# Kernel tuning notes

Hardware: AMD Instinct MI355X
Metric: run time of the kernel (lower is better)

The kernel has to match this reference:

```python
import jax, jax.numpy as jnp
import numpy as np
import math

D_MODEL = 512
EXPAND = 2
D_INNER = EXPAND * D_MODEL          # 1024
HEADDIM = 8
NHEADS = D_INNER // HEADDIM         # 128
NGROUPS = 2
D_STATE = 16
CONV_DIM = D_INNER + 2 * NGROUPS * D_STATE   # 1088
D_IN_PROJ = 2 * D_INNER + 2 * NGROUPS * D_STATE + NHEADS  # 2240
P13 = [(0, 0), (1, 1)]
P31 = [(1, 1), (0, 0)]
P33 = [(1, 1), (1, 1)]


def silu(x):
    return x * jax.nn.sigmoid(x)


def dwconv(x, w, pad):
    # depthwise 2D conv; x: (B,C,H,W), w: (C,1,kh,kw)
    return jax.lax.conv_general_dilated(
        x, w, (1, 1), pad,
        dimension_numbers=('NCHW', 'OIHW', 'NCHW'),
        feature_group_count=x.shape[1])


def interleave_ch(a, b):
    # channel-interleave: out[:, ::2] = a, out[:, 1::2] = b
    Bn, C, Hh, Ww = a.shape
    return jnp.stack([a, b], axis=2).reshape(Bn, 2 * C, Hh, Ww)


def linear_attn(x, dt, A, Bm, Cm, Dp):
    # non-causal linear-attention duality of Mamba2 (grouped heads)
    # x: (B,L,h,p), dt: (B,L,h), A: (h,) negative, Bm/Cm: (B,L,g*ds), Dp: (h,)
    b, L, h, p = x.shape
    g, ds = NGROUPS, D_STATE
    dA = -(dt * A[None, None, :])          # ssd_positive_dA -> positive
    Vs = x * dA[..., None]
    K = Bm.reshape(b, L, g, ds)
    Q = Cm.reshape(b, L, g, ds)
    Vg = Vs.reshape(b, L, h // g, g, p)
    KV = jnp.einsum('blgs,blmgp->bmgsp', K, Vg)       # (b, h/g, g, ds, p)
    y = jnp.einsum('blgs,bmgsp->blmgp', Q, KV)        # (b, L, h/g, g, p)
    y = y + (x * Dp[None, None, :, None]).reshape(b, L, h // g, g, p)
    return y.reshape(b, L, h, p)


def setup_inputs() -> dict:
    key = jax.random.key(0)
    ks = jax.random.split(key, 20)
    Bn, Hh, Ww = 8, 64, 64
    L = Hh * Ww
    u = jax.random.normal(ks[0], (Bn, L, D_MODEL), jnp.float32)
    W_in = jax.random.normal(ks[1], (D_IN_PROJ, D_MODEL), jnp.float32) / math.sqrt(D_MODEL)
    dt = jnp.exp(jax.random.uniform(ks[2], (NHEADS,)) * (math.log(0.1) - math.log(0.001)) + math.log(0.001))
    dt = jnp.clip(dt, 1e-4, None)
    dt_bias = dt + jnp.log(-jnp.expm1(-dt))
    A_log = jnp.log(jax.random.uniform(ks[3], (NHEADS,), minval=1.0, maxval=16.0))
    Dp = jnp.ones((NHEADS,), jnp.float32)

    def cw(k, c, kh, kw):
        return jax.random.normal(k, (c, 1, kh, kw), jnp.float32) / math.sqrt(kh * kw)

    bcC = 2 * NGROUPS * D_STATE // 4  # 16
    w_conv2d = cw(ks[4], CONV_DIM // 2, 3, 3)
    w13x1 = cw(ks[5], D_INNER // 4, 1, 3)
    w31x1 = cw(ks[6], D_INNER // 4, 3, 1)
    w13x2 = cw(ks[7], D_INNER // 4, 1, 3)
    w31x2 = cw(ks[8], D_INNER // 4, 3, 1)
    w13bc1 = cw(ks[9], bcC, 1, 3)
    w31bc1 = cw(ks[10], bcC, 3, 1)
    w13bc2 = cw(ks[11], bcC, 1, 3)
    w31bc2 = cw(ks[12], bcC, 3, 1)
    w_conv2d_z = cw(ks[13], D_INNER, 3, 3)
    ln_g = jnp.ones((D_INNER,), jnp.float32)
    ln_b = jnp.zeros((D_INNER,), jnp.float32)
    scale = jnp.float32(1.0)
    shift = jnp.float32(0.0)
    alpha1 = jnp.float32(1.0)
    alpha2 = jnp.float32(1.0)
    W_out = jax.random.normal(ks[14], (D_MODEL, 2 * D_INNER), jnp.float32) / math.sqrt(2 * D_INNER)
    return dict(u=u, H=Hh, W=Ww, W_in=W_in, dt_bias=dt_bias, A_log=A_log, Dp=Dp,
                w_conv2d=w_conv2d, w13x1=w13x1, w31x1=w31x1, w13x2=w13x2, w31x2=w31x2,
                w13bc1=w13bc1, w31bc1=w31bc1, w13bc2=w13bc2, w31bc2=w31bc2,
                w_conv2d_z=w_conv2d_z, ln_g=ln_g, ln_b=ln_b, scale=scale, shift=shift,
                alpha1=alpha1, alpha2=alpha2, W_out=W_out)


def reference(u, H, W, W_in, dt_bias, A_log, Dp, w_conv2d, w13x1, w31x1, w13x2, w31x2,
              w13bc1, w31bc1, w13bc2, w31bc2, w_conv2d_z, ln_g, ln_b, scale, shift,
              alpha1, alpha2, W_out):
    Bn, L, _ = u.shape
    zxbcdt = u @ W_in.T                                 # (B,L,2240)
    z = zxbcdt[..., :D_INNER]
    xBC = zxbcdt[..., D_INNER:D_INNER + CONV_DIM]
    dt = zxbcdt[..., D_INNER + CONV_DIM:]
    dt = jax.nn.softplus(dt + dt_bias)                  # (B,L,h)

    # even/odd channel-interleave split, reshape to NCHW feature maps
    even = xBC[..., 0::2].reshape(Bn, H, W, -1).transpose(0, 3, 1, 2)
    odd = xBC[..., 1::2].reshape(Bn, H, W, -1).transpose(0, 3, 1, 2)
    even = silu(dwconv(even, w_conv2d, P33))

    oe = odd[:, 0::2]
    oo = odd[:, 1::2]
    x_oe, bc_oe = oe[:, :D_INNER // 4], oe[:, D_INNER // 4:]
    x_oo, bc_oo = oo[:, :D_INNER // 4], oo[:, D_INNER // 4:]
    x_oe = silu(dwconv(dwconv(x_oe, w31x1, P31), w13x1, P13))
    x_oo = silu(dwconv(dwconv(x_oo, w13x2, P13), w31x2, P31))
    bc_oe = silu(dwconv(dwconv(bc_oe, w13bc1, P13), w31bc1, P31))
    bc_oo = silu(dwconv(dwconv(bc_oo, w31bc2, P31), w13bc2, P13))
    xbc_oe = jnp.concatenate([x_oe, bc_oe], axis=1)
    xbc_oo = jnp.concatenate([x_oo, bc_oo], axis=1)
    odd = interleave_ch(xbc_oe, xbc_oo)

    xBCc = interleave_ch(even, odd)                     # (B, CONV_DIM, H, W)
    xBCc = xBCc.transpose(0, 2, 3, 1).reshape(Bn, L, CONV_DIM)
    x = xBCc[..., :D_INNER]
    Bm = xBCc[..., D_INNER:D_INNER + NGROUPS * D_STATE]
    Cm = xBCc[..., D_INNER + NGROUPS * D_STATE:]

    A = -jnp.exp(A_log)
    y = linear_attn(x.reshape(Bn, L, NHEADS, HEADDIM), dt, A, Bm, Cm, Dp)
    y = y.reshape(Bn, L, D_INNER)

    mu = y.mean(-1, keepdims=True)
    var = ((y - mu) ** 2).mean(-1, keepdims=True)
    y = (y - mu) / jnp.sqrt(var + 1e-5) * ln_g + ln_b
    y = y * scale + shift

    zc = z.reshape(Bn, H, W, D_INNER).transpose(0, 3, 1, 2)
    zc = silu(dwconv(zc, w_conv2d_z, P33))
    zc = zc.transpose(0, 2, 3, 1).reshape(Bn, L, D_INNER)

    out = jnp.concatenate([alpha1 * y, alpha2 * zc], axis=-1) @ W_out.T
    return out
```

## Files before the change

### kernel.cpp

```cpp
#include <hip/hip_runtime.h>
#include <hip/hip_bf16.h>
#include <cstdint>
#include <cstddef>

#define HDIM    64
#define WDIM    64
#define LPB     4096
#define DMODEL  512
#define DIN     1024
#define CONVD   1088
#define DPROJ   2240
#define NHEADS  128
#define NCV     2112

using f16    = _Float16;
using f16x4  = __attribute__((ext_vector_type(4))) _Float16;
using f16x8  = __attribute__((ext_vector_type(8))) _Float16;
using f32x4  = __attribute__((ext_vector_type(4))) float;

#define VM_CNT(n) asm volatile("s_waitcnt vmcnt(" #n ")" ::: "memory")
#define LDSFENCE  asm volatile("" ::: "memory")

__device__ __forceinline__ float siluf(float x) { return x / (1.f + __expf(-x)); }
__device__ __forceinline__ float fsilu(float x) {
  return x * __builtin_amdgcn_rcpf(1.f + __expf(-x));
}

__device__ __forceinline__ void fma_mix_lo(float& acc, unsigned a, unsigned b) {
  asm("v_fma_mix_f32 %0, %1, %2, %0 op_sel_hi:[1,1,0]" : "+v"(acc) : "v"(a), "v"(b));
}
__device__ __forceinline__ void fma_mix_hi(float& acc, unsigned a, unsigned b) {
  asm("v_fma_mix_f32 %0, %1, %2, %0 op_sel:[1,1,0] op_sel_hi:[1,1,0]" : "+v"(acc) : "v"(a), "v"(b));
}
__device__ __forceinline__ void fmixl(float& acc, unsigned a, float b) {
  asm("v_fma_mix_f32 %0, %1, %2, %0 op_sel_hi:[1,0,0]" : "+v"(acc) : "v"(a), "v"(b));
}
__device__ __forceinline__ void fmixh(float& acc, unsigned a, float b) {
  asm("v_fma_mix_f32 %0, %1, %2, %0 op_sel:[1,0,0] op_sel_hi:[1,0,0]" : "+v"(acc) : "v"(a), "v"(b));
}
__device__ __forceinline__ void fma8(float* acc, const uint4& v, const uint4& w) {
  fma_mix_lo(acc[0], v.x, w.x);  fma_mix_hi(acc[1], v.x, w.x);
  fma_mix_lo(acc[2], v.y, w.y);  fma_mix_hi(acc[3], v.y, w.y);
  fma_mix_lo(acc[4], v.z, w.z);  fma_mix_hi(acc[5], v.z, w.z);
  fma_mix_lo(acc[6], v.w, w.w);  fma_mix_hi(acc[7], v.w, w.w);
}

__global__ __launch_bounds__(256) void k_cvt(const float* __restrict__ in, f16* __restrict__ out) {
  size_t i = ((size_t)blockIdx.x * 256 + threadIdx.x) * 4;
  f32x4 v = *(const f32x4*)(in + i);
  f16x4 o;
  #pragma unroll
  for (int j = 0; j < 4; ++j) o[j] = (f16)v[j];
  *(f16x4*)(out + i) = o;
}

__global__ __launch_bounds__(256) void k_cvt_win(const float* __restrict__ W, f16* __restrict__ out) {
  int i = blockIdx.x * 256 + threadIdx.x;
  int row = i >> 9, col = i & 511;
  float v = (row < DPROJ) ? W[row * 512 + col] : 0.f;
  out[i] = (f16)v;
}

__global__ __launch_bounds__(256) void k_keff(const float* __restrict__ w33,
                       const float* __restrict__ w13x1, const float* __restrict__ w31x1,
                       const float* __restrict__ w13x2, const float* __restrict__ w31x2,
                       const float* __restrict__ w13bc1, const float* __restrict__ w31bc1,
                       const float* __restrict__ w13bc2, const float* __restrict__ w31bc2,
                       const float* __restrict__ wz,
                       f16* __restrict__ keffall) {
  int j = blockIdx.x * 256 + threadIdx.x;
  if (j >= NCV) return;
  if (j < 1024) {
    #pragma unroll
    for (int tap = 0; tap < 9; ++tap) keffall[tap * NCV + j] = (f16)wz[j * 9 + tap];
    return;
  }
  int jj = j - 1024;
  float kh[3] = {0,0,0}, kw[3] = {0,0,0};
  bool dense = ((jj & 1) == 0);
  if (!dense) {
    int m = jj >> 2;
    if ((jj & 3) == 1) {
      if (m < 256) { for (int t=0;t<3;++t){ kh[t]=w31x1[m*3+t];  kw[t]=w13x1[m*3+t];  } }
      else { int q=m-256; for (int t=0;t<3;++t){ kh[t]=w31bc1[q*3+t]; kw[t]=w13bc1[q*3+t]; } }
    } else {
      if (m < 256) { for (int t=0;t<3;++t){ kh[t]=w31x2[m*3+t];  kw[t]=w13x2[m*3+t];  } }
      else { int q=m-256; for (int t=0;t<3;++t){ kh[t]=w31bc2[q*3+t]; kw[t]=w13bc2[q*3+t]; } }
    }
  }
  #pragma unroll
  for (int dh = 0; dh < 3; ++dh)
    #pragma unroll
    for (int dw = 0; dw < 3; ++dw) {
      float v = dense ? w33[(jj >> 1) * 9 + dh*3 + dw] : kh[dh] * kw[dw];
      keffall[(dh*3 + dw) * NCV + j] = (f16)v;
    }
}

__global__ __launch_bounds__(512, 1) void k_gemm8(const f16* __restrict__ A, int lda,
                                                  const f16* __restrict__ Bm, int ldb,
                                                  f16* __restrict__ C, int ldc,
                                                  int K, int NW, int ntn) {
  __shared__ __align__(16) f16 Al[2 * 16384];
  __shared__ __align__(16) f16 Bl[2 * 16384];

  int nwg = gridDim.x, bid = blockIdx.x;
  int q = nwg >> 3, r = nwg & 7;
  int xcd = bid & 7, loc = bid >> 3;
  int wg  = (xcd < r ? xcd * (q + 1) : r * (q + 1) + (xcd - r) * q) + loc;
  long m0 = (long)(wg / ntn) * 256;
  long n0 = (long)(wg % ntn) * 256;

  const int tid  = threadIdx.x;
  const int wid  = tid >> 6, lane = tid & 63;
  const int wr   = wid >> 2, wc = wid & 3;

  const int rowoff = wid * 8 + (lane >> 3);
  const int scolS  = ((lane & 7) ^ (lane >> 3)) * 8;
  const int ldst   = wid * 512;

  const int fr   = lane & 15;
  const int koff = (lane >> 4) * 8;
  const int swz8 = (lane & 7) << 3;

  f32x4 acc[8][4];
  #pragma unroll
  for (int i = 0; i < 8; ++i)
    #pragma unroll
    for (int j = 0; j < 4; ++j) acc[i][j] = (f32x4){0.f,0.f,0.f,0.f};

  const int NT = K >> 6;

  auto stA = [&](int par, int X, int kb) {
    __builtin_amdgcn_global_load_lds(
      (const __attribute__((address_space(1))) void*)(A + (m0 + X*64 + rowoff) * (long)lda + kb + scolS),
      (__attribute__((address_space(3))) void*)&Al[par*16384 + X*4096 + ldst], 16, 0, 0);
  };
  auto stB = [&](int par, int X, int kb) {
    __builtin_amdgcn_global_load_lds(
      (const __attribute__((address_space(1))) void*)(Bm + (n0 + X*64 + rowoff) * (long)ldb + kb + scolS),
      (__attribute__((address_space(3))) void*)&Bl[par*16384 + X*4096 + ldst], 16, 0, 0);
  };

  stB(0,0,0); stB(0,1,0); stB(0,2,0); stB(0,3,0);
  stA(0,0,0); stA(0,2,0); stA(0,1,0); stA(0,3,0);

  for (int t = 0; t < NT; ++t) {
    const bool last = (t == NT - 1);
    const int pr = t & 1, pw = (t + 1) & 1;
    const int kb = (t + 1) << 6;
    const f16* Ard = &Al[pr * 16384];
    const f16* Brd = &Bl[pr * 16384];
    f16x8 bf[4][2];

    #pragma unroll
    for (int s = 0; s < 4; ++s) {
      f16x8 af[2][2];
      if (s == 1 || s == 3) {
        #pragma unroll
        for (int j = 0; j < 2; ++j)
          #pragma unroll
          for (int k = 0; k < 2; ++k) {
            int rr = wr*128 + (2*s + j)*16 + fr;
            af[j][k] = *(const f16x8*)&Ard[rr*64 + ((k*32 + koff) ^ swz8)];
          }
      }
      if (!last) {
        if (s == 0)      { stB(pw, 0, kb); stB(pw, 1, kb); }
        else if (s == 1) { stB(pw, 2, kb); stB(pw, 3, kb); }
        else if (s == 2) { stA(pw, 0, kb); stA(pw, 2, kb); }
        else             { stA(pw, 1, kb); stA(pw, 3, kb); }
      }
      if (s == 0) { if (!last) { VM_CNT(4); } else { VM_CNT(2); } }
      if (s == 2) { if (!last) { VM_CNT(6); } else { VM_CNT(0); } }
      __builtin_amdgcn_s_barrier();
      LDSFENCE;
      if (s == 0) {
        #pragma unroll
        for (int ni = 0; ni < 4; ++ni)
          #pragma unroll
          for (int k = 0; k < 2; ++k) {
            int rr = wc*64 + ni*16 + fr;
            bf[ni][k] = *(const f16x8*)&Brd[rr*64 + ((k*32 + koff) ^ swz8)];
          }
      }
      if (s == 0 || s == 2) {
        #pragma unroll
        for (int j = 0; j < 2; ++j)
          #pragma unroll
          for (int k = 0; k < 2; ++k) {
            int rr = wr*128 + (2*s + j)*16 + fr;
            af[j][k] = *(const f16x8*)&Ard[rr*64 + ((k*32 + koff) ^ swz8)];
          }
      }
      __builtin_amdgcn_s_setprio(1);
      #pragma unroll
      for (int j = 0; j < 2; ++j)
        #pragma unroll
        for (int ni = 0; ni < 4; ++ni)
          #pragma unroll
          for (int k = 0; k < 2; ++k)
            acc[2*s + j][ni] = __builtin_amdgcn_mfma_f32_16x16x32_f16(af[j][k], bf[ni][k], acc[2*s + j][ni], 0, 0, 0);
      __builtin_amdgcn_s_setprio(0);
      __builtin_amdgcn_s_barrier();
      LDSFENCE;
    }
  }

  const int cr = (lane >> 4) * 4;
  const int cc = lane & 15;
  #pragma unroll
  for (int mi = 0; mi < 8; ++mi) {
    long rbase = m0 + wr*128 + mi*16 + cr;
    #pragma unroll
    for (int ni = 0; ni < 4; ++ni) {
      int col = (int)n0 + wc*64 + ni*16 + cc;
      if (col < NW) {
        f16* cp = C + rbase * (long)ldc + col;
        #pragma unroll
        for (int rr2 = 0; rr2 < 4; ++rr2) cp[(long)rr2 * ldc] = (f16)acc[mi][ni][rr2];
      }
    }
  }
}

template<typename OutT>
__global__ __launch_bounds__(256) void k_gemmf(const f16* __restrict__ A, int lda,
                                               const f16* __restrict__ Bm, int ldb,
                                               OutT* __restrict__ C, int ldc,
                                               int Kseg, int NW, int ntn, int ntmn, long Cseg) {
  __shared__ __align__(16) f16 As[128 * 32];
  __shared__ __align__(16) f16 Bs[128 * 32];

  int nwg = gridDim.x, bid = blockIdx.x;
  int q = nwg >> 3, r = nwg & 7;
  int xcd = bid & 7, loc = bid >> 3;
  int wg  = (xcd < r ? xcd * (q + 1) : r * (q + 1) + (xcd - r) * q) + loc;
  int kseg = wg / ntmn;
  int rem  = wg - kseg * ntmn;
  long m0 = (long)(rem / ntn) * 128;
  long n0 = (long)(rem % ntn) * 128;
  const int kbase = kseg * Kseg;

  const int tid  = threadIdx.x;
  const int w    = tid >> 6, lane = tid & 63;
  const int wr   = w >> 1, wc = w & 1;

  f32x4 acc[4][4];
  #pragma unroll
  for (int i = 0; i < 4; ++i)
    #pragma unroll
    for (int j = 0; j < 4; ++j) acc[i][j] = (f32x4){0.f,0.f,0.f,0.f};

  const int srow = w * 16 + (lane >> 2);
  const int scol = (lane & 3) * 8;
  const long aoff = (m0 + srow) * (long)lda + scol + kbase;
  const long boff = (n0 + srow) * (long)ldb + scol + kbase;
  const int fr = lane & 15;
  const int kc = (lane >> 4) * 8;

  for (int k0 = 0; k0 < Kseg; k0 += 32) {
    #pragma unroll
    for (int i = 0; i < 2; ++i) {
      long ao = aoff + (long)i*64*lda + k0;
      long bo = boff + (long)i*64*ldb + k0;
      int ls = (i*4 + w) * 512;
      __builtin_amdgcn_global_load_lds((const __attribute__((address_space(1))) void*)(A + ao),
                                       (__attribute__((address_space(3))) void*)&As[ls], 16, 0, 0);
      __builtin_amdgcn_global_load_lds((const __attribute__((address_space(1))) void*)(Bm + bo),
                                       (__attribute__((address_space(3))) void*)&Bs[ls], 16, 0, 0);
    }
    __syncthreads();
    f16x8 af[4], bf[4];
    #pragma unroll
    for (int f = 0; f < 4; ++f) {
      af[f] = *(const f16x8*)&As[(wr*64 + f*16 + fr) * 32 + kc];
      bf[f] = *(const f16x8*)&Bs[(wc*64 + f*16 + fr) * 32 + kc];
    }
    #pragma unroll
    for (int i = 0; i < 4; ++i)
      #pragma unroll
      for (int j = 0; j < 4; ++j)
        acc[i][j] = __builtin_amdgcn_mfma_f32_16x16x32_f16(af[i], bf[j], acc[i][j], 0, 0, 0);
    __syncthreads();
  }

  OutT* Cb = C + (long)kseg * Cseg;
  const int cr = (lane >> 4) * 4;
  const int cc = lane & 15;
  #pragma unroll
  for (int i = 0; i < 4; ++i) {
    long rbase = m0 + wr*64 + i*16 + cr;
    #pragma unroll
    for (int j = 0; j < 4; ++j) {
      int col = (int)n0 + wc*64 + j*16 + cc;
      if (col < NW) {
        OutT* cp = Cb + rbase * (long)ldc + col;
        #pragma unroll
        for (int r2 = 0; r2 < 4; ++r2) cp[(long)r2 * ldc] = (OutT)acc[i][j][r2];
      }
    }
  }
}

__global__ __launch_bounds__(256) void k_red2h(const f16* __restrict__ part, long seg,
                                               float* __restrict__ out) {
  long i = ((long)blockIdx.x * 256 + threadIdx.x) * 4;
  f16x4 s0 = *(const f16x4*)(part + i);
  f16x4 s1 = *(const f16x4*)(part + seg + i);
  f32x4 o;
  #pragma unroll
  for (int j = 0; j < 4; ++j) o[j] = (float)s0[j] + (float)s1[j];
  *(f32x4*)(out + i) = o;
}

__global__ __launch_bounds__(192) void k_conv_all(const f16* __restrict__ zx,
                                                  const f16* __restrict__ keffall,
                                                  const float* __restrict__ a2_p,
                                                  const float* __restrict__ dt_bias,
                                                  const float* __restrict__ A_log,
                                                  f16* __restrict__ xbc,
                                                  f16* __restrict__ g2,
                                                  float* __restrict__ dAb) {
  int t = threadIdx.x;
  int bid = blockIdx.x, qq = gridDim.x >> 3;
  int grp = (bid & 7) * qq + (bid >> 3);
  int l0 = grp * 2;
  long lb = (long)(l0 & ~(LPB - 1));
  int h  = (l0 >> 6) & 63;
  int w0 = l0 & 63;

  if (t < 132) {
    int c0 = t * 8;
    int c1 = c0 + 1056;
    float a00[8] = {0,0,0,0,0,0,0,0};
    float a01[8] = {0,0,0,0,0,0,0,0};
    float a10[8] = {0,0,0,0,0,0,0,0};
    float a11[8] = {0,0,0,0,0,0,0,0};
    const uint4 z4 = {0u,0u,0u,0u};

    #pragma unroll
    for (int dh = 0; dh < 3; ++dh) {
      int hh = h + dh - 1;
      if (hh < 0 || hh >= HDIM) continue;
      const f16* rp = zx + (lb + (long)(hh * 64)) * DPROJ;
      uint4 v0[4], v1[4];
      #pragma unroll
      for (int pp = 0; pp < 4; ++pp) {
        int ww = w0 + pp - 1;
        ww = ww < 0 ? 0 : (ww > 63 ? 63 : ww);
        const f16* tp = rp + (long)ww * DPROJ;
        v0[pp] = *(const uint4*)(tp + c0);
        v1[pp] = *(const uint4*)(tp + c1);
      }
      if (w0 == 0)  { v0[0] = z4; v1[0] = z4; }
      if (w0 == 62) { v0[3] = z4; v1[3] = z4; }
      #pragma unroll
      for (int dw = 0; dw < 3; ++dw) {
        uint4 wa = *(const uint4*)&keffall[(dh*3 + dw) * NCV + c0];
        uint4 wb = *(const uint4*)&keffall[(dh*3 + dw) * NCV + c1];
        fma8(a00, v0[dw],     wa);
        fma8(a10, v0[dw + 1], wa);
        fma8(a01, v1[dw],     wb);
        fma8(a11, v1[dw + 1], wb);
      }
    }

    float a2 = a2_p[0];
    #pragma unroll
    for (int ti = 0; ti < 2; ++ti) {
      long l = l0 + ti;
      const float* pc0 = ti ? a10 : a00;
      const float* pc1 = ti ? a11 : a01;
      f16x8 o8;
      if (c0 < 1024) {
        #pragma unroll
        for (int j = 0; j < 8; ++j) o8[j] = (f16)(a2 * fsilu(pc0[j]));
        *(f16x8*)&g2[l * 2048 + 1024 + c0] = o8;
      } else {
        #pragma unroll
        for (int j = 0; j < 8; ++j) o8[j] = (f16)fsilu(pc0[j]);
        *(f16x8*)&xbc[l * (long)CONVD + (c0 - 1024)] = o8;
      }
      f16x8 o9;
      #pragma unroll
      for (int j = 0; j < 8; ++j) o9[j] = (f16)fsilu(pc1[j]);
      *(f16x8*)&xbc[l * (long)CONVD + (c1 - 1024)] = o9;
    }
  } else if (t < 164) {
    int idx = t - 132;
    int ti = idx >> 4;
    int hd = (idx & 15) * 8;
    long l = l0 + ti;
    f16x8 x = *(const f16x8*)&zx[l * (long)DPROJ + NCV + hd];
    f32x4 o0, o1;
    #pragma unroll
    for (int j = 0; j < 8; ++j) {
      float xx = (float)x[j] + dt_bias[hd + j];
      float sp = (xx > 20.f) ? xx : log1pf(__expf(xx));
      float dv = sp * __expf(A_log[hd + j]);
      if (j < 4) o0[j] = dv; else o1[j-4] = dv;
    }
    *(f32x4*)&dAb[l * 128 + hd]     = o0;
    *(f32x4*)&dAb[l * 128 + hd + 4] = o1;
  }
}

__global__ __launch_bounds__(512) void k_kv_part(const f16* __restrict__ xbc,
                                                 const float* __restrict__ dA,
                                                 float* __restrict__ part) {
  int t = threadIdx.x;
  int m = t >> 3, p = t & 7;
  int lc = blockIdx.x, b = blockIdx.y;
  float acc0[16], acc1[16];
  #pragma unroll
  for (int s = 0; s < 16; ++s) { acc0[s] = 0.f; acc1[s] = 0.f; }
  long lbase = (long)b * LPB + lc * 64;
  for (int li = 0; li < 64; li += 2) {
    long row = lbase + li;
    const f16* xr0 = xbc + row * CONVD;
    const f16* xr1 = xr0 + CONVD;
    float2 aa0 = *(const float2*)&dA[row * 128 + 2*m];
    float2 aa1 = *(const float2*)&dA[(row + 1) * 128 + 2*m];
    f16 x00s = xr0[16*m + p],     x01s = xr0[16*m + 8 + p];
    f16 x10s = xr1[16*m + p],     x11s = xr1[16*m + 8 + p];
    uint4 q00 = *(const uint4*)(xr0 + DIN);
    uint4 q01 = *(const uint4*)(xr0 + DIN + 8);
    uint4 q02 = *(const uint4*)(xr0 + DIN + 16);
    uint4 q03 = *(const uint4*)(xr0 + DIN + 24);
    uint4 q10 = *(const uint4*)(xr1 + DIN);
    uint4 q11 = *(const uint4*)(xr1 + DIN + 8);
    uint4 q12 = *(const uint4*)(xr1 + DIN + 16);
    uint4 q13 = *(const uint4*)(xr1 + DIN + 24);
    float xv00 = (float)x00s * aa0.x, xv01 = (float)x01s * aa0.y;
    float xv10 = (float)x10s * aa1.x, xv11 = (float)x11s * aa1.y;
    unsigned a00[4] = {q00.x, q00.y, q00.z, q00.w};
    unsigned a01[4] = {q01.x, q01.y, q01.z, q01.w};
    unsigned a02[4] = {q02.x, q02.y, q02.z, q02.w};
    unsigned a03[4] = {q03.x, q03.y, q03.z, q03.w};
    unsigned a10[4] = {q10.x, q10.y, q10.z, q10.w};
    unsigned a11[4] = {q11.x, q11.y, q11.z, q11.w};
    unsigned a12[4] = {q12.x, q12.y, q12.z, q12.w};
    unsigned a13[4] = {q13.x, q13.y, q13.z, q13.w};
    #pragma unroll
    for (int k = 0; k < 4; ++k) {
      fmixl(acc0[2*k],   a00[k], xv00);  fmixh(acc0[2*k+1],   a00[k], xv00);
      fmixl(acc0[8+2*k], a01[k], xv00);  fmixh(acc0[8+2*k+1], a01[k], xv00);
      fmixl(acc1[2*k],   a02[k], xv01);  fmixh(acc1[2*k+1],   a02[k], xv01);
      fmixl(acc1[8+2*k], a03[k], xv01);  fmixh(acc1[8+2*k+1], a03[k], xv01);
      fmixl(acc0[2*k],   a10[k], xv10);  fmixh(acc0[2*k+1],   a10[k], xv10);
      fmixl(acc0[8+2*k], a11[k], xv10);  fmixh(acc0[8+2*k+1], a11[k], xv10);
      fmixl(acc1[2*k],   a12[k], xv11);  fmixh(acc1[2*k+1],   a12[k], xv11);
      fmixl(acc1[8+2*k], a13[k], xv11);  fmixh(acc1[8+2*k+1], a13[k], xv11);
    }
  }
  long base = ((long)(b*64 + lc)) * 16384 + (long)m * 256;
  #pragma unroll
  for (int s = 0; s < 16; ++s) {
    part[base + s*8 + p]       = acc0[s];
    part[base + 128 + s*8 + p] = acc1[s];
  }
}

__global__ __launch_bounds__(256) void k_kv_red(const float* __restrict__ part,
                                                float* __restrict__ KV) {
  int e4 = (blockIdx.x * 256 + threadIdx.x) * 4;
  int b = blockIdx.y;
  f32x4 s = (f32x4){0.f,0.f,0.f,0.f};
  #pragma unroll 4
  for (int lc = 0; lc < 64; ++lc) {
    f32x4 v = *(const f32x4*)&part[((long)(b*64 + lc)) * 16384 + e4];
    #pragma unroll
    for (int j = 0; j < 4; ++j) s[j] += v[j];
  }
  *(f32x4*)&KV[(long)b * 16384 + e4] = s;
}

__global__ __launch_bounds__(256) void k_y_ln(const f16* __restrict__ xbc,
                                              const float* __restrict__ KV,
                                              const float* __restrict__ Dp,
                                              const float* __restrict__ ln_g,
                                              const float* __restrict__ ln_b,
                                              const float* __restrict__ sc_p,
                                              const float* __restrict__ sh_p,
                                              const float* __restrict__ a1_p,
                                              f16* __restrict__ g2) {
  __shared__ float Qs[64][32];
  __shared__ float red[2][2][8];
  int t = threadIdx.x;
  int hd = t >> 1, pb = (t & 1) * 4;
  int m = hd >> 1, g = hd & 1;
  int b = blockIdx.x >> 6;
  long l0 = (long)b * LPB + (blockIdx.x & 63) * 64;

  f32x4 kv[16];
  #pragma unroll
  for (int s = 0; s < 16; ++s)
    kv[s] = *(const f32x4*)&KV[(long)b * 16384 + m*256 + g*128 + s*8 + pb];

  {
    int tok = t >> 2, q8 = (t & 3) * 8;
    f16x8 qv = *(const f16x8*)&xbc[(l0 + tok) * CONVD + 1056 + q8];
    #pragma unroll
    for (int j = 0; j < 8; ++j) Qs[tok][q8 + j] = (float)qv[j];
  }
  int c0 = hd*8 + pb;
  f32x4 lg = *(const f32x4*)&ln_g[c0];
  f32x4 lb = *(const f32x4*)&ln_b[c0];
  float dpv = Dp[hd];
  float sc = sc_p[0], sh = sh_p[0], a1 = a1_p[0];
  int wv = t >> 6, lane = t & 63;
  __syncthreads();

  for (int tok = 0; tok < 64; tok += 2) {
    int par = (tok >> 1) & 1;
    long row0 = l0 + tok, row1 = row0 + 1;
    f16x4 xa = *(const f16x4*)&xbc[row0 * CONVD + c0];
    f16x4 xb = *(const f16x4*)&xbc[row1 * CONVD + c0];
    f32x4 ya, yb;
    #pragma unroll
    for (int j = 0; j < 4; ++j) { ya[j] = (float)xa[j] * dpv; yb[j] = (float)xb[j] * dpv; }
    #pragma unroll
    for (int s = 0; s < 16; ++s) {
      float qa = Qs[tok][g*16 + s];
      float qb = Qs[tok + 1][g*16 + s];
      #pragma unroll
      for (int j = 0; j < 4; ++j) {
        ya[j] = fmaf(qa, kv[s][j], ya[j]);
        yb[j] = fmaf(qb, kv[s][j], yb[j]);
      }
    }
    float s1a = ya[0]+ya[1]+ya[2]+ya[3];
    float s2a = ya[0]*ya[0]+ya[1]*ya[1]+ya[2]*ya[2]+ya[3]*ya[3];
    float s1b = yb[0]+yb[1]+yb[2]+yb[3];
    float s2b = yb[0]*yb[0]+yb[1]*yb[1]+yb[2]*yb[2]+yb[3]*yb[3];
    #pragma unroll
    for (int off = 1; off < 64; off <<= 1) {
      s1a += __shfl_xor(s1a, off, 64);
      s2a += __shfl_xor(s2a, off, 64);
      s1b += __shfl_xor(s1b, off, 64);
      s2b += __shfl_xor(s2b, off, 64);
    }
    if (lane == 0) {
      red[par][0][wv*2] = s1a;  red[par][0][wv*2 + 1] = s2a;
      red[par][1][wv*2] = s1b;  red[par][1][wv*2 + 1] = s2b;
    }
    __syncthreads();
    #pragma unroll
    for (int ti = 0; ti < 2; ++ti) {
      const float* rr = red[par][ti];
      float S1 = rr[0] + rr[2] + rr[4] + rr[6];
      float S2 = rr[1] + rr[3] + rr[5] + rr[7];
      float mu   = S1 * (1.f/1024.f);
      float var  = S2 * (1.f/1024.f) - mu*mu;
      float rstd = rsqrtf(var + 1e-5f);
      f32x4& yv = ti ? yb : ya;
      f16x4 o4;
      #pragma unroll
      for (int j = 0; j < 4; ++j) {
        float yn = (yv[j] - mu) * rstd * lg[j] + lb[j];
        o4[j] = (f16)(a1 * (yn * sc + sh));
      }
      *(f16x4*)&g2[(l0 + tok + ti) * 2048 + c0] = o4;
    }
  }
}

extern "C" void kernel_launch(void* const* d_in, const int* in_sizes, int n_in,
                              void* d_out, int out_size, void* d_ws, size_t ws_size,
                              hipStream_t stream) {
  const float* u       = (const float*)d_in[0];
  const float* W_in    = (const float*)d_in[3];
  const float* dt_bias = (const float*)d_in[4];
  const float* A_log   = (const float*)d_in[5];
  const float* Dp      = (const float*)d_in[6];
  const float* w33     = (const float*)d_in[7];
  const float* w13x1   = (const float*)d_in[8];
  const float* w31x1   = (const float*)d_in[9];
  const float* w13x2   = (const float*)d_in[10];
  const float* w31x2   = (const float*)d_in[11];
  const float* w13bc1  = (const float*)d_in[12];
  const float* w31bc1  = (const float*)d_in[13];
  const float* w13bc2  = (const float*)d_in[14];
  const float* w31bc2  = (const float*)d_in[15];
  const float* wz      = (const float*)d_in[16];
  const float* ln_g    = (const float*)d_in[17];
  const float* ln_b    = (const float*)d_in[18];
  const float* sc      = (const float*)d_in[19];
  const float* sh      = (const float*)d_in[20];
  const float* a1      = (const float*)d_in[21];
  const float* a2      = (const float*)d_in[22];
  const float* W_out   = (const float*)d_in[23];

  const size_t B_G2   = 16777216;
  const size_t B_ZX   = 18350080;
  const size_t B_XBC  = 8912896;
  const size_t B_DA   = 2097152;
  const size_t B_KV   = 65536;
  const size_t perC   = B_G2 + B_ZX + B_XBC + B_DA + B_KV;
  const size_t persist = 2359296 + 2097152 + 38912;

  int C = 8;
  while (C > 1 && persist + (size_t)C * perC > ws_size) C >>= 1;
  const int nch = 8 / C;
  const int Mc  = C * LPB;

  char* p = (char*)d_ws;
  f16*   win_f   = (f16*)p;   p += 2359296;
  f16*   wout_f  = (f16*)p;   p += 2097152;
  f16*   keffall = (f16*)p;   p += 38912;
  char*  arena   = p;
  f16*   g2      = (f16*)arena;
  f16*   u_f     = (f16*)arena;
  p = arena + (size_t)C * B_G2;
  f16*   zx      = (f16*)p;   p += (size_t)C * B_ZX;
  f16*   xbc     = (f16*)p;   p += (size_t)C * B_XBC;
  float* dAb     = (float*)p; p += (size_t)C * B_DA;
  float* KV      = (float*)p; p += (size_t)C * B_KV;
  float* part   = (float*)zx;
  f16*   kpart  = (f16*)zx;

  k_cvt_win<<<4608, 256, 0, stream>>>(W_in, win_f);
  k_cvt    <<<1024, 256, 0, stream>>>(W_out, wout_f);
  k_keff   <<<9, 256, 0, stream>>>(w33, w13x1, w31x1, w13x2, w31x2,
                                   w13bc1, w31bc1, w13bc2, w31bc2, wz, keffall);

  for (int ch = 0; ch < nch; ++ch) {
    const float* uc   = u + (size_t)ch * Mc * 512;
    float*       outc = (float*)d_out + (size_t)ch * Mc * 512;
    const int ntm = Mc / 128;

    k_cvt<<<Mc/2, 256, 0, stream>>>(uc, u_f);

    k_gemm8<<<(Mc/256)*9, 512, 0, stream>>>(u_f, 512, win_f, 512,
                                            zx, DPROJ, 512, DPROJ, 9);

    k_conv_all<<<Mc/2, 192, 0, stream>>>(zx, keffall, a2, dt_bias, A_log,
                                         xbc, g2, dAb);

    k_kv_part <<<dim3(64, C), 512, 0, stream>>>(xbc, dAb, part);
    k_kv_red  <<<dim3(16, C), 256, 0, stream>>>(part, KV);
    k_y_ln    <<<C*64, 256, 0, stream>>>(xbc, KV, Dp, ln_g, ln_b, sc, sh, a1, g2);

    const long cseg = (long)Mc * 512;
    k_gemmf<f16><<<ntm*4*2, 256, 0, stream>>>(g2, 2048, wout_f, 2048,
                                              kpart, 512, 1024, 512, 4, ntm*4, cseg);
    k_red2h<<<Mc/2, 256, 0, stream>>>(kpart, cseg, outc);
  }
}
```

Before: 546.6 us.

## Fuse fp32-to-fp16 input conversion into a smaller-tile in-projection GEMM

Drops the separate pass that converts the fp32 input u to fp16. The in-projection GEMM now loads fp32 A tiles straight into LDS and converts them to fp16 in registers before the MFMAs. The large 256x256 tile, double-buffered, software-pipelined kernel is replaced by a simple 128x128 single-buffered kernel with K-step 32 and two barriers per step. This saves one extra read and write of the activations, but loses the load/compute overlap, doubles A traffic by loading fp32, and adds conversion work in the inner loop.

```diff
diff --git a/kernel.cpp b/kernel.cpp
--- a/kernel.cpp
+++ b/kernel.cpp
@@ -17,9 +17,6 @@
 using f16x4  = __attribute__((ext_vector_type(4))) _Float16;
 using f16x8  = __attribute__((ext_vector_type(8))) _Float16;
 using f32x4  = __attribute__((ext_vector_type(4))) float;
-
-#define VM_CNT(n) asm volatile("s_waitcnt vmcnt(" #n ")" ::: "memory")
-#define LDSFENCE  asm volatile("" ::: "memory")
 
 __device__ __forceinline__ float siluf(float x) { return x / (1.f + __expf(-x)); }
 __device__ __forceinline__ float fsilu(float x) {
@@ -97,128 +94,81 @@
     }
 }
 
-__global__ __launch_bounds__(512, 1) void k_gemm8(const f16* __restrict__ A, int lda,
-                                                  const f16* __restrict__ Bm, int ldb,
-                                                  f16* __restrict__ C, int ldc,
-                                                  int K, int NW, int ntn) {
-  __shared__ __align__(16) f16 Al[2 * 16384];
-  __shared__ __align__(16) f16 Bl[2 * 16384];
+__global__ __launch_bounds__(256) void k_gemm1c(const float* __restrict__ A,
+                                                const f16* __restrict__ Bm, int ldb,
+                                                f16* __restrict__ C, int ldc,
+                                                int K, int NW, int ntn) {
+  __shared__ __align__(16) float As[128 * 32];
+  __shared__ __align__(16) f16   Bs[128 * 32];
 
   int nwg = gridDim.x, bid = blockIdx.x;
   int q = nwg >> 3, r = nwg & 7;
   int xcd = bid & 7, loc = bid >> 3;
   int wg  = (xcd < r ? xcd * (q + 1) : r * (q + 1) + (xcd - r) * q) + loc;
-  long m0 = (long)(wg / ntn) * 256;
-  long n0 = (long)(wg % ntn) * 256;
+  long m0 = (long)(wg / ntn) * 128;
+  long n0 = (long)(wg % ntn) * 128;
 
   const int tid  = threadIdx.x;
-  const int wid  = tid >> 6, lane = tid & 63;
-  const int wr   = wid >> 2, wc = wid & 3;
-
-  const int rowoff = wid * 8 + (lane >> 3);
-  const int scolS  = ((lane & 7) ^ (lane >> 3)) * 8;
-  const int ldst   = wid * 512;
-
+  const int w    = tid >> 6, lane = tid & 63;
+  const int wr   = w >> 1, wc = w & 1;
+
+  f32x4 acc[4][4];
+  #pragma unroll
+  for (int i = 0; i < 4; ++i)
+    #pragma unroll
+    for (int j = 0; j < 4; ++j) acc[i][j] = (f32x4){0.f,0.f,0.f,0.f};
+
+  const int arow = tid >> 3;
+  const int acol = (tid & 7) * 4;
+  const int brow = w * 16 + (lane >> 2);
+  const int bcol = (lane & 3) * 8;
   const int fr   = lane & 15;
-  const int koff = (lane >> 4) * 8;
-  const int swz8 = (lane & 7) << 3;
-
-  f32x4 acc[8][4];
-  #pragma unroll
-  for (int i = 0; i < 8; ++i)
-    #pragma unroll
-    for (int j = 0; j < 4; ++j) acc[i][j] = (f32x4){0.f,0.f,0.f,0.f};
-
-  const int NT = K >> 6;
-
-  auto stA = [&](int par, int X, int kb) {
-    __builtin_amdgcn_global_load_lds(
-      (const __attribute__((address_space(1))) void*)(A + (m0 + X*64 + rowoff) * (long)lda + kb + scolS),
-      (__attribute__((address_space(3))) void*)&Al[par*16384 + X*4096 + ldst], 16, 0, 0);
-  };
-  auto stB = [&](int par, int X, int kb) {
-    __builtin_amdgcn_global_load_lds(
-      (const __attribute__((address_space(1))) void*)(Bm + (n0 + X*64 + rowoff) * (long)ldb + kb + scolS),
-      (__attribute__((address_space(3))) void*)&Bl[par*16384 + X*4096 + ldst], 16, 0, 0);
-  };
-
-  stB(0,0,0); stB(0,1,0); stB(0,2,0); stB(0,3,0);
-  stA(0,0,0); stA(0,2,0); stA(0,1,0); stA(0,3,0);
-
-  for (int t = 0; t < NT; ++t) {
-    const bool last = (t == NT - 1);
-    const int pr = t & 1, pw = (t + 1) & 1;
-    const int kb = (t + 1) << 6;
-    const f16* Ard = &Al[pr * 16384];
-    const f16* Brd = &Bl[pr * 16384];
-    f16x8 bf[4][2];
-
-    #pragma unroll
-    for (int s = 0; s < 4; ++s) {
-      f16x8 af[2][2];
-      if (s == 1 || s == 3) {
-        #pragma unroll
-        for (int j = 0; j < 2; ++j)
-          #pragma unroll
-          for (int k = 0; k < 2; ++k) {
-            int rr = wr*128 + (2*s + j)*16 + fr;
-            af[j][k] = *(const f16x8*)&Ard[rr*64 + ((k*32 + koff) ^ swz8)];
-          }
-      }
-      if (!last) {
-        if (s == 0)      { stB(pw, 0, kb); stB(pw, 1, kb); }
-        else if (s == 1) { stB(pw, 2, kb); stB(pw, 3, kb); }
-        else if (s == 2) { stA(pw, 0, kb); stA(pw, 2, kb); }
-        else             { stA(pw, 1, kb); stA(pw, 3, kb); }
-      }
-      if (s == 0) { if (!last) { VM_CNT(4); } else { VM_CNT(2); } }
-      if (s == 2) { if (!last) { VM_CNT(6); } else { VM_CNT(0); } }
-      __builtin_amdgcn_s_barrier();
-      LDSFENCE;
-      if (s == 0) {
-        #pragma unroll
-        for (int ni = 0; ni < 4; ++ni)
-          #pragma unroll
-          for (int k = 0; k < 2; ++k) {
-            int rr = wc*64 + ni*16 + fr;
-            bf[ni][k] = *(const f16x8*)&Brd[rr*64 + ((k*32 + koff) ^ swz8)];
-          }
-      }
-      if (s == 0 || s == 2) {
-        #pragma unroll
-        for (int j = 0; j < 2; ++j)
-          #pragma unroll
-          for (int k = 0; k < 2; ++k) {
-            int rr = wr*128 + (2*s + j)*16 + fr;
-            af[j][k] = *(const f16x8*)&Ard[rr*64 + ((k*32 + koff) ^ swz8)];
-          }
-      }
-      __builtin_amdgcn_s_setprio(1);
-      #pragma unroll
-      for (int j = 0; j < 2; ++j)
-        #pragma unroll
-        for (int ni = 0; ni < 4; ++ni)
-          #pragma unroll
-          for (int k = 0; k < 2; ++k)
-            acc[2*s + j][ni] = __builtin_amdgcn_mfma_f32_16x16x32_f16(af[j][k], bf[ni][k], acc[2*s + j][ni], 0, 0, 0);
-      __builtin_amdgcn_s_setprio(0);
-      __builtin_amdgcn_s_barrier();
-      LDSFENCE;
-    }
+  const int kc   = (lane >> 4) * 8;
+
+  for (int k0 = 0; k0 < K; k0 += 32) {
+    #pragma unroll
+    for (int i = 0; i < 4; ++i) {
+      __builtin_amdgcn_global_load_lds(
+        (const __attribute__((address_space(1))) void*)(A + (m0 + i*32 + arow) * 512L + acol + k0),
+        (__attribute__((address_space(3))) void*)&As[(i*256 + tid) * 4], 16, 0, 0);
+    }
+    #pragma unroll
+    for (int i = 0; i < 2; ++i) {
+      __builtin_amdgcn_global_load_lds(
+        (const __attribute__((address_space(1))) void*)(Bm + (n0 + i*64 + brow) * (long)ldb + bcol + k0),
+        (__attribute__((address_space(3))) void*)&Bs[(i*4 + w) * 512], 16, 0, 0);
+    }
+    __syncthreads();
+    f16x8 af[4], bf[4];
+    #pragma unroll
+    for (int f = 0; f < 4; ++f) {
+      int rr = wr*64 + f*16 + fr;
+      f32x4 a0 = *(const f32x4*)&As[rr*32 + kc];
+      f32x4 a1 = *(const f32x4*)&As[rr*32 + kc + 4];
+      #pragma unroll
+      for (int j = 0; j < 4; ++j) { af[f][j] = (f16)a0[j]; af[f][4+j] = (f16)a1[j]; }
+      bf[f] = *(const f16x8*)&Bs[(wc*64 + f*16 + fr) * 32 + kc];
+    }
+    #pragma unroll
+    for (int i = 0; i < 4; ++i)
+      #pragma unroll
+      for (int j = 0; j < 4; ++j)
+        acc[i][j] = __builtin_amdgcn_mfma_f32_16x16x32_f16(af[i], bf[j], acc[i][j], 0, 0, 0);
+    __syncthreads();
   }
 
   const int cr = (lane >> 4) * 4;
   const int cc = lane & 15;
   #pragma unroll
-  for (int mi = 0; mi < 8; ++mi) {
-    long rbase = m0 + wr*128 + mi*16 + cr;
-    #pragma unroll
-    for (int ni = 0; ni < 4; ++ni) {
-      int col = (int)n0 + wc*64 + ni*16 + cc;
+  for (int i = 0; i < 4; ++i) {
+    long rbase = m0 + wr*64 + i*16 + cr;
+    #pragma unroll
+    for (int j = 0; j < 4; ++j) {
+      int col = (int)n0 + wc*64 + j*16 + cc;
       if (col < NW) {
         f16* cp = C + rbase * (long)ldc + col;
         #pragma unroll
-        for (int rr2 = 0; rr2 < 4; ++rr2) cp[(long)rr2 * ldc] = (f16)acc[mi][ni][rr2];
+        for (int r2 = 0; r2 < 4; ++r2) cp[(long)r2 * ldc] = (f16)acc[i][j][r2];
       }
     }
   }
@@ -609,10 +559,7 @@
   f16*   win_f   = (f16*)p;   p += 2359296;
   f16*   wout_f  = (f16*)p;   p += 2097152;
   f16*   keffall = (f16*)p;   p += 38912;
-  char*  arena   = p;
-  f16*   g2      = (f16*)arena;
-  f16*   u_f     = (f16*)arena;
-  p = arena + (size_t)C * B_G2;
+  f16*   g2      = (f16*)p;   p += (size_t)C * B_G2;
   f16*   zx      = (f16*)p;   p += (size_t)C * B_ZX;
   f16*   xbc     = (f16*)p;   p += (size_t)C * B_XBC;
   float* dAb     = (float*)p; p += (size_t)C * B_DA;
@@ -630,10 +577,7 @@
     float*       outc = (float*)d_out + (size_t)ch * Mc * 512;
     const int ntm = Mc / 128;
 
-    k_cvt<<<Mc/2, 256, 0, stream>>>(uc, u_f);
-
-    k_gemm8<<<(Mc/256)*9, 512, 0, stream>>>(u_f, 512, win_f, 512,
-                                            zx, DPROJ, 512, DPROJ, 9);
+    k_gemm1c<<<ntm*18, 256, 0, stream>>>(uc, win_f, 512, zx, DPROJ, 512, DPROJ, 18);
 
     k_conv_all<<<Mc/2, 192, 0, stream>>>(zx, keffall, a2, dt_bias, A_log,
                                          xbc, g2, dAb);
```

Result: slower. 564.5 us (+3.3%).
